# Performance work log

Measured on AMD Instinct MI355X. Metric: run time of the kernel, lower is better.

Reference implementation:

```python
import jax, jax.numpy as jnp
import numpy as np

N_NODES = 100000
N_EDGES = 1000000
N_GRAPHS = 2048
IN_DIM, HIDDEN, OUT_DIM = 5, 64, 128


def setup_inputs() -> dict:
    key = jax.random.key(0)
    ks = jax.random.split(key, 12)
    x = jax.random.normal(ks[0], (N_NODES, IN_DIM), dtype=jnp.float32)
    edge_index = jax.random.randint(ks[1], (2, N_EDGES), 0, N_NODES, dtype=jnp.int64)
    batch = jnp.sort(jax.random.randint(ks[2], (N_NODES,), 0, N_GRAPHS, dtype=jnp.int64))
    def lin(k, fan_in, fan_out):
        bound = 1.0 / np.sqrt(fan_in)
        kw, kb = jax.random.split(k)
        W = jax.random.uniform(kw, (fan_in, fan_out), jnp.float32, -bound, bound)
        b = jax.random.uniform(kb, (fan_out,), jnp.float32, -bound, bound)
        return W, b
    W1, b1 = lin(ks[3], IN_DIM, HIDDEN)
    W2, b2 = lin(ks[4], HIDDEN, HIDDEN)
    W3, b3 = lin(ks[5], HIDDEN, HIDDEN)
    W4, b4 = lin(ks[6], HIDDEN, OUT_DIM)
    return {"x": x, "edge_index": edge_index, "batch": batch,
            "W1": W1, "b1": b1, "W2": W2, "b2": b2,
            "W3": W3, "b3": b3, "W4": W4, "b4": b4}


def _gcn_conv(x, W, b, src, dst, norm, n):
    # h = x W; message from src, scaled by symmetric norm, scattered to dst
    h = x @ W                                   # [N, F]
    msg = h[src] * norm[:, None]                # [E+N, F] gather
    agg = jax.ops.segment_sum(msg, dst, num_segments=n)  # scatter-add
    return agg + b


def reference(x, edge_index, batch, W1, b1, W2, b2, W3, b3, W4, b4):
    n = x.shape[0]
    loop = jnp.arange(n, dtype=edge_index.dtype)
    # GCN with self-loops: src -> dst aggregation, D^-1/2 A_hat D^-1/2 norm
    src = jnp.concatenate([edge_index[0], loop])
    dst = jnp.concatenate([edge_index[1], loop])
    deg = jax.ops.segment_sum(jnp.ones_like(dst, dtype=x.dtype), dst, num_segments=n)
    dinv = jnp.where(deg > 0, jax.lax.rsqrt(jnp.maximum(deg, 1.0)), 0.0)
    norm = dinv[src] * dinv[dst]                # [E+N]

    h = jax.nn.relu(_gcn_conv(x, W1, b1, src, dst, norm, n))
    h = jax.nn.relu(_gcn_conv(h, W2, b2, src, dst, norm, n))

    # global mean pool per graph
    sums = jax.ops.segment_sum(h, batch, num_segments=N_GRAPHS)      # [G, F]
    cnts = jax.ops.segment_sum(jnp.ones((n,), h.dtype), batch, num_segments=N_GRAPHS)
    pooled = sums / jnp.maximum(cnts, 1.0)[:, None]

    # MLP head
    z = jax.nn.relu(pooled @ W3 + b3)
    return z @ W4 + b4
```

## Files before the change

kernel.cpp:

```cpp
#include <hip/hip_runtime.h>
#include <hip/hip_fp16.h>

#define N_NODES  100000
#define N_EDGES  1000000
#define N_GRAPHS 2048
#define IN_DIM   5
#define HIDDEN   64
#define OUT_DIM  128
#define CAP      32
#define NA       512
#define PART     256
#define NBIN     391
#define CAPBIN   4096
#define LSTR     72
#define MAXN     192
#define NSTG     96
#define EPT      8

typedef _Float16 f16x8 __attribute__((ext_vector_type(8)));
typedef float    f32x4 __attribute__((ext_vector_type(4)));


__global__ void __launch_bounds__(256) k_part2(
        const int* __restrict__ src, const int* __restrict__ dst,
        const int* __restrict__ batch, int* __restrict__ gcursor,
        int* __restrict__ epart, int* __restrict__ gs) {
    __shared__ int h[NBIN];
    __shared__ int off[NBIN];
    int t = threadIdx.x, b = blockIdx.x;

    int gid = b * 256 + t;
    if (gid < N_NODES) {
        int bi = batch[gid];
        int bp = (gid == 0) ? -1 : batch[gid - 1];
        for (int g = bp + 1; g <= bi; g++) gs[g] = gid;
        if (gid == N_NODES - 1)
            for (int g = bi + 1; g <= N_GRAPHS; g++) gs[g] = N_NODES;
    }

    for (int i = t; i < NBIN; i += 256) h[i] = 0;
    __syncthreads();
    int ebin[EPT], epay[EPT];
    int ebase = b * 256 + t;
#pragma unroll
    for (int i = 0; i < EPT; i++) {
        int e = ebase + i * (NA * 256);
        ebin[i] = -1;
        if (e < N_EDGES) {
            int d = dst[e];
            ebin[i] = d >> 8;
            epay[i] = ((d & (PART - 1)) << 17) | src[e];
            atomicAdd(&h[ebin[i]], 1);
        }
    }
    __syncthreads();
    for (int i = t; i < NBIN; i += 256) {
        int c = h[i];
        int base = c ? atomicAdd(&gcursor[i], c) : 0;
        off[i] = i * CAPBIN + base;
    }
    __syncthreads();
#pragma unroll
    for (int i = 0; i < EPT; i++) {
        if (ebin[i] >= 0) {
            int pos = atomicAdd(&off[ebin[i]], 1);
            if (pos < (ebin[i] + 1) * CAPBIN)
                epart[pos] = epay[i];
        }
    }
}

__global__ void __launch_bounds__(256) k_build(
        const int* __restrict__ epart, const int* __restrict__ bincnt,
        const float* __restrict__ x, int* __restrict__ cnt, int* __restrict__ bkt,
        float* __restrict__ dinv, __half* __restrict__ xs) {
    __shared__ int lcnt[PART];
    __shared__ int lrows[PART * CAP];
    int t = threadIdx.x, b = blockIdx.x;
    int base = b * PART;
    for (int i = t; i < PART; i += 256) lcnt[i] = 0;
    __syncthreads();
    int estart = b * CAPBIN;
    int eend = estart + min(bincnt[b], CAPBIN);
    for (int i = estart + t; i < eend; i += 256) {
        int ed = epart[i];
        int ln = ed >> 17;
        int c = atomicAdd(&lcnt[ln], 1);
        if (c < CAP) lrows[ln * CAP + c] = ed & 0x1FFFF;
    }
    __syncthreads();
    int gbase = base * CAP;
    int lim = min(PART * CAP, N_NODES * CAP - gbase);
    for (int i = t; i < lim; i += 256) bkt[gbase + i] = lrows[i];
    for (int n = t; n < PART; n += 256) {
        int g = base + n;
        if (g < N_NODES) {
            int c = lcnt[n];
            cnt[g] = c;
            float d = rsqrtf(1.0f + (float)c);
            dinv[g] = d;
            union { __half h[8]; float4 f4; } u;
#pragma unroll
            for (int k = 0; k < 8; k++)
                u.h[k] = __float2half((k < IN_DIM) ? x[g * IN_DIM + k] * d : 0.0f);
            ((float4*)xs)[g] = u.f4;
        }
    }
}

__global__ void __launch_bounds__(256) k_g5l12(
        const int* __restrict__ cnt, const int* __restrict__ bkt,
        const __half* __restrict__ xs,
        const float* __restrict__ W1, const float* __restrict__ b1,
        const float* __restrict__ W2, const float* __restrict__ dinv,
        __half* __restrict__ hs2h) {
    __shared__ __align__(16) _Float16 lh1[64 * LSTR];
    __shared__ __align__(16) _Float16 lw2[64 * LSTR];
    __shared__ float la5[64][8];
    __shared__ unsigned short ordn[64];
    __shared__ int dsh[CAP + 1];
    __shared__ int sdeg[64];
    int tid = threadIdx.x;
    int w = tid >> 6, l = tid & 63;
    int nodeBase = blockIdx.x * 64;

#pragma unroll
    for (int i = 0; i < 4; i++) {
        int idx = tid + i * 256;
        float4 wv = ((const float4*)W2)[idx];
        int k = idx >> 4, n4 = (idx & 15) * 4;
        lw2[(n4 + 0) * LSTR + k] = (_Float16)wv.x;
        lw2[(n4 + 1) * LSTR + k] = (_Float16)wv.y;
        lw2[(n4 + 2) * LSTR + k] = (_Float16)wv.z;
        lw2[(n4 + 3) * LSTR + k] = (_Float16)wv.w;
    }

    int* sbkt5 = (int*)lh1;
    {
        const int4* gb = (const int4*)(bkt + (size_t)nodeBase * CAP);
        int4* sb = (int4*)sbkt5;
        int lim4 = min(64, N_NODES - nodeBase) * (CAP / 4);
        for (int i = tid; i < lim4; i += 256) sb[i] = gb[i];
    }

    if (tid <= CAP) dsh[tid] = 0;
    __syncthreads();
    int mydeg = 0;
    if (tid < 64) {
        int g = nodeBase + tid;
        mydeg = (g < N_NODES) ? min(cnt[g], CAP) : 0;
        sdeg[tid] = mydeg;
        atomicAdd(&dsh[mydeg], 1);
    }
    __syncthreads();
    if (tid < 64) {
        int orig = (tid <= CAP) ? dsh[tid] : 0;
        int v = orig;
#pragma unroll
        for (int off = 1; off < 64; off <<= 1) {
            int u = __shfl_up(v, off);
            if (tid >= off) v += u;
        }
        if (tid <= CAP) dsh[tid] = v - orig;
    }
    __syncthreads();
    if (tid < 64) { int pos = atomicAdd(&dsh[mydeg], 1); ordn[pos] = tid; }
    __syncthreads();

    {
        int g4 = l >> 2, l4 = l & 3;
        int lnm = ordn[w * 16 + g4];
        int g = nodeBase + lnm;
        float s0 = 0.f, s1 = 0.f, s2 = 0.f, s3 = 0.f;
        float s4 = 0.f, s5 = 0.f, s6 = 0.f, s7 = 0.f;
        if (g < N_NODES) {
            const float4* XS4 = (const float4*)xs;
            int len = sdeg[lnm];
            const int* row = sbkt5 + lnm * CAP;
#define XACC(r) { const __half2* hp_ = (const __half2*)&(r);                   \
            float2 u0_ = __half22float2(hp_[0]), u1_ = __half22float2(hp_[1]); \
            float2 u2_ = __half22float2(hp_[2]), u3_ = __half22float2(hp_[3]); \
            s0 += u0_.x; s1 += u0_.y; s2 += u1_.x; s3 += u1_.y;                \
            s4 += u2_.x; s5 += u2_.y; s6 += u3_.x; s7 += u3_.y; }
            int e = l4;
            for (; e + 4 < len; e += 8) {
                float4 r0 = XS4[row[e]];
                float4 r1 = XS4[row[e + 4]];
                XACC(r0); XACC(r1);
            }
            if (e < len) { float4 r0 = XS4[row[e]]; XACC(r0); }
            if (l4 == 0) { float4 rs = XS4[g]; XACC(rs); }
#undef XACC
        }
#pragma unroll
        for (int m = 1; m <= 2; m <<= 1) {
            s0 += __shfl_xor(s0, m); s1 += __shfl_xor(s1, m);
            s2 += __shfl_xor(s2, m); s3 += __shfl_xor(s3, m);
            s4 += __shfl_xor(s4, m); s5 += __shfl_xor(s5, m);
            s6 += __shfl_xor(s6, m); s7 += __shfl_xor(s7, m);
        }
        if (l4 == 0) {
            float d = (g < N_NODES) ? dinv[g] : 0.f;
            la5[lnm][0] = s0 * d; la5[lnm][1] = s1 * d;
            la5[lnm][2] = s2 * d; la5[lnm][3] = s3 * d;
            la5[lnm][4] = s4 * d; la5[lnm][5] = s5 * d;
            la5[lnm][6] = s6 * d; la5[lnm][7] = s7 * d;
        }
    }
    __syncthreads();

    int f = l;
    float b1v = b1[f];
    float w1v[IN_DIM];
#pragma unroll
    for (int k = 0; k < IN_DIM; k++) w1v[k] = W1[k * HIDDEN + f];
    for (int i = 0; i < 16; i++) {
        int ln = w * 16 + i;
        float t1 = b1v;
#pragma unroll
        for (int k = 0; k < IN_DIM; k++)
            t1 += la5[ln][k] * w1v[k];
        lh1[ln * LSTR + f] = (_Float16)fmaxf(t1, 0.f);
    }
    __syncthreads();

    int quad = l >> 4, m16 = l & 15;
    f32x4 acc0 = {0.f, 0.f, 0.f, 0.f};
    f32x4 acc1 = {0.f, 0.f, 0.f, 0.f};
    f32x4 acc2 = {0.f, 0.f, 0.f, 0.f};
    f32x4 acc3 = {0.f, 0.f, 0.f, 0.f};
#pragma unroll
    for (int kc = 0; kc < 2; kc++) {
        f16x8 a = *(const f16x8*)&lh1[(w * 16 + m16) * LSTR + kc * 32 + quad * 8];
        f16x8 b0 = *(const f16x8*)&lw2[(0 * 16 + m16) * LSTR + kc * 32 + quad * 8];
        f16x8 b1f = *(const f16x8*)&lw2[(1 * 16 + m16) * LSTR + kc * 32 + quad * 8];
        f16x8 b2 = *(const f16x8*)&lw2[(2 * 16 + m16) * LSTR + kc * 32 + quad * 8];
        f16x8 b3 = *(const f16x8*)&lw2[(3 * 16 + m16) * LSTR + kc * 32 + quad * 8];
        acc0 = __builtin_amdgcn_mfma_f32_16x16x32_f16(a, b0, acc0, 0, 0, 0);
        acc1 = __builtin_amdgcn_mfma_f32_16x16x32_f16(a, b1f, acc1, 0, 0, 0);
        acc2 = __builtin_amdgcn_mfma_f32_16x16x32_f16(a, b2, acc2, 0, 0, 0);
        acc3 = __builtin_amdgcn_mfma_f32_16x16x32_f16(a, b3, acc3, 0, 0, 0);
    }
#pragma unroll
    for (int i = 0; i < 4; i++) {
        int g = nodeBase + w * 16 + quad * 4 + i;
        if (g >= N_NODES) continue;
        float dv = dinv[g];
        __half* row = hs2h + (size_t)g * HIDDEN + m16;
        row[0]  = __float2half(acc0[i] * dv);
        row[16] = __float2half(acc1[i] * dv);
        row[32] = __float2half(acc2[i] * dv);
        row[48] = __float2half(acc3[i] * dv);
    }
}

__global__ void __launch_bounds__(256) k_g2ph(
        const int* __restrict__ cnt, const int* __restrict__ bkt,
        const __half* __restrict__ hs2h, const float* __restrict__ dinv,
        const int* __restrict__ gs, const float* __restrict__ b2,
        const float* __restrict__ W3, const float* __restrict__ b3,
        const float* __restrict__ W4, const float* __restrict__ b4,
        float* __restrict__ out) {
    __shared__ __align__(16) int sbkt[NSTG][CAP];
    __shared__ int   scnt[NSTG];
    __shared__ float sdinv[NSTG];
    __shared__ float pool[4][HIDDEN];
    __shared__ float gp[HIDDEN];
    __shared__ float gz[HIDDEN];
    __shared__ unsigned short ord[MAXN];
    __shared__ int dsh[CAP + 1];
    int g = blockIdx.x, tid = threadIdx.x;
    int grp = tid >> 3, l8 = tid & 7;
    int w = tid >> 6;
    int s = gs[g], e = gs[g + 1];
    int n = e - s;
    int nst = min(n, NSTG);
    bool dosort = (n <= MAXN);

    {
        const int4* gb = (const int4*)(bkt + (size_t)s * CAP);
        int4* sb = (int4*)&sbkt[0][0];
        int tot = nst * (CAP / 4);
        for (int i = tid; i < tot; i += 256) sb[i] = gb[i];
    }
    for (int i = tid; i < nst; i += 256) {
        scnt[i]  = min(cnt[s + i], CAP);
        sdinv[i] = dinv[s + i];
    }
    if (tid <= CAP) dsh[tid] = 0;
    __syncthreads();

    int mydeg = 0;
    if (dosort && tid < n) {
        mydeg = (tid < nst) ? scnt[tid] : min(cnt[s + tid], CAP);
        atomicAdd(&dsh[mydeg], 1);
    }
    __syncthreads();
    if (tid < 64) {
        int orig = (tid <= CAP) ? dsh[tid] : 0;
        int v = orig;
#pragma unroll
        for (int off = 1; off < 64; off <<= 1) {
            int u = __shfl_up(v, off);
            if (tid >= off) v += u;
        }
        if (tid <= CAP) dsh[tid] = v - orig;
    }
    __syncthreads();
    if (dosort && tid < n) { int pos = atomicAdd(&dsh[mydeg], 1); ord[pos] = tid; }
    __syncthreads();

    const float4* H16 = (const float4*)hs2h;
    float4 b2a = ((const float4*)b2)[l8 * 2];
    float4 b2b = ((const float4*)b2)[l8 * 2 + 1];
    float p0 = 0.f, p1 = 0.f, p2 = 0.f, p3 = 0.f;
    float p4 = 0.f, p5 = 0.f, p6 = 0.f, p7 = 0.f;

#define ACCA(r) { const __half2* hp_ = (const __half2*)&(r);               \
        float2 u0_ = __half22float2(hp_[0]), u1_ = __half22float2(hp_[1]); \
        float2 u2_ = __half22float2(hp_[2]), u3_ = __half22float2(hp_[3]); \
        a0 += u0_.x; a1 += u0_.y; a2 += u1_.x; a3 += u1_.y;                \
        a4 += u2_.x; a5 += u2_.y; a6 += u3_.x; a7 += u3_.y; }
#define ACCC(r) { const __half2* hp_ = (const __half2*)&(r);               \
        float2 u0_ = __half22float2(hp_[0]), u1_ = __half22float2(hp_[1]); \
        float2 u2_ = __half22float2(hp_[2]), u3_ = __half22float2(hp_[3]); \
        c0 += u0_.x; c1 += u0_.y; c2 += u1_.x; c3 += u1_.y;                \
        c4 += u2_.x; c5 += u2_.y; c6 += u3_.x; c7 += u3_.y; }

#define NODE_BODY(ROW, LEN, DV, NODE)                                      \
    {                                                                      \
        float a0 = 0.f, a1 = 0.f, a2 = 0.f, a3 = 0.f;                      \
        float a4 = 0.f, a5 = 0.f, a6 = 0.f, a7 = 0.f;                      \
        float c0 = 0.f, c1 = 0.f, c2 = 0.f, c3 = 0.f;                      \
        float c4 = 0.f, c5 = 0.f, c6 = 0.f, c7 = 0.f;                      \
        int ee = 0;                                                        \
        for (; ee + 8 <= (LEN); ee += 8) {                                 \
            int4 i0 = *(const int4*)&(ROW)[ee];                            \
            int4 i1 = *(const int4*)&(ROW)[ee + 4];                        \
            float4 r0 = H16[(size_t)i0.x * 8 + l8];                        \
            float4 r1 = H16[(size_t)i0.y * 8 + l8];                        \
            float4 r2 = H16[(size_t)i0.z * 8 + l8];                        \
            float4 r3 = H16[(size_t)i0.w * 8 + l8];                        \
            float4 r4 = H16[(size_t)i1.x * 8 + l8];                        \
            float4 r5 = H16[(size_t)i1.y * 8 + l8];                        \
            float4 r6 = H16[(size_t)i1.z * 8 + l8];                        \
            float4 r7 = H16[(size_t)i1.w * 8 + l8];                        \
            ACCA(r0); ACCC(r1); ACCA(r2); ACCC(r3);                        \
            ACCA(r4); ACCC(r5); ACCA(r6); ACCC(r7);                        \
        }                                                                  \
        if (ee + 4 <= (LEN)) {                                             \
            int4 i0 = *(const int4*)&(ROW)[ee];                            \
            float4 r0 = H16[(size_t)i0.x * 8 + l8];                        \
            float4 r1 = H16[(size_t)i0.y * 8 + l8];                        \
            float4 r2 = H16[(size_t)i0.z * 8 + l8];                        \
            float4 r3 = H16[(size_t)i0.w * 8 + l8];                        \
            ACCA(r0); ACCC(r1); ACCA(r2); ACCC(r3);                        \
            ee += 4;                                                       \
        }                                                                  \
        for (; ee < (LEN); ee++) {                                         \
            float4 r0 = H16[(size_t)(ROW)[ee] * 8 + l8];                   \
            ACCA(r0);                                                      \
        }                                                                  \
        { float4 rs = H16[(size_t)(NODE) * 8 + l8]; ACCA(rs); }            \
        float dv_ = (DV);                                                  \
        p0 += fmaxf((a0 + c0) * dv_ + b2a.x, 0.f);                         \
        p1 += fmaxf((a1 + c1) * dv_ + b2a.y, 0.f);                         \
        p2 += fmaxf((a2 + c2) * dv_ + b2a.z, 0.f);                         \
        p3 += fmaxf((a3 + c3) * dv_ + b2a.w, 0.f);                         \
        p4 += fmaxf((a4 + c4) * dv_ + b2b.x, 0.f);                         \
        p5 += fmaxf((a5 + c5) * dv_ + b2b.y, 0.f);                         \
        p6 += fmaxf((a6 + c6) * dv_ + b2b.z, 0.f);                         \
        p7 += fmaxf((a7 + c7) * dv_ + b2b.w, 0.f);                         \
    }

    if (n <= NSTG) {
        for (int r = grp; r < n; r += 32) {
            int ln = dosort ? (int)ord[r] : r;
            const int* row = &sbkt[ln][0];
            NODE_BODY(row, scnt[ln], sdinv[ln], s + ln);
        }
    } else {
        for (int r = grp; r < n; r += 32) {
            int ln = dosort ? (int)ord[r] : r;
            int node = s + ln;
            const int* row = bkt + (size_t)node * CAP;
            NODE_BODY(row, min(cnt[node], CAP), dinv[node], node);
        }
    }
#undef NODE_BODY
#undef ACCA
#undef ACCC
#pragma unroll
    for (int m = 8; m <= 32; m <<= 1) {
        p0 += __shfl_xor(p0, m); p1 += __shfl_xor(p1, m);
        p2 += __shfl_xor(p2, m); p3 += __shfl_xor(p3, m);
        p4 += __shfl_xor(p4, m); p5 += __shfl_xor(p5, m);
        p6 += __shfl_xor(p6, m); p7 += __shfl_xor(p7, m);
    }
    if ((tid & 63) < 8) {
        float* pw = &pool[w][l8 * 8];
        pw[0] = p0; pw[1] = p1; pw[2] = p2; pw[3] = p3;
        pw[4] = p4; pw[5] = p5; pw[6] = p6; pw[7] = p7;
    }
    __syncthreads();
    if (tid < HIDDEN) {
        float inv = 1.0f / fmaxf((float)n, 1.0f);
        gp[tid] = (pool[0][tid] + pool[1][tid] + pool[2][tid] + pool[3][tid]) * inv;
    }
    __syncthreads();
    if (tid < HIDDEN) {
        float t = b3[tid];
#pragma unroll 8
        for (int k = 0; k < HIDDEN; k++) t += gp[k] * W3[k * HIDDEN + tid];
        gz[tid] = fmaxf(t, 0.f);
    }
    __syncthreads();
    if (tid < OUT_DIM) {
        float t = b4[tid];
#pragma unroll 8
        for (int k = 0; k < HIDDEN; k++) t += gz[k] * W4[k * OUT_DIM + tid];
        out[(size_t)g * OUT_DIM + tid] = t;
    }
}

extern "C" void kernel_launch(void* const* d_in, const int* in_sizes, int n_in,
                              void* d_out, int out_size, void* d_ws, size_t ws_size,
                              hipStream_t stream) {
    const float* x  = (const float*)d_in[0];
    const int*   ei = (const int*)d_in[1];
    const int*   batch = (const int*)d_in[2];
    const float* W1 = (const float*)d_in[3];
    const float* b1 = (const float*)d_in[4];
    const float* W2 = (const float*)d_in[5];
    const float* b2 = (const float*)d_in[6];
    const float* W3 = (const float*)d_in[7];
    const float* b3 = (const float*)d_in[8];
    const float* W4 = (const float*)d_in[9];
    const float* b4 = (const float*)d_in[10];
    float* out = (float*)d_out;

    const int* src = ei;
    const int* dst = ei + N_EDGES;

    char* wp = (char*)d_ws;
    auto carve = [&](size_t bytes) -> void* {
        void* p = (void*)wp;
        wp += (bytes + 255) & ~(size_t)255;
        return p;
    };
    int*    cnt     = (int*)carve((size_t)N_NODES * sizeof(int));
    int*    bkt     = (int*)carve((size_t)N_NODES * CAP * sizeof(int));
    float*  dinv    = (float*)carve((size_t)N_NODES * sizeof(float));
    __half* hs2h    = (__half*)carve((size_t)N_NODES * HIDDEN * sizeof(__half));
    __half* xs      = (__half*)carve((size_t)N_NODES * 8 * sizeof(__half));
    int*    epart   = (int*)carve((size_t)NBIN * CAPBIN * sizeof(int));
    int*    gs      = (int*)carve((size_t)(N_GRAPHS + 1) * sizeof(int));
    int*    gcursor = (int*)carve((size_t)NBIN * sizeof(int));

    hipMemsetAsync(gcursor, 0, (size_t)NBIN * sizeof(int), stream);
    k_part2<<<NA, 256, 0, stream>>>(src, dst, batch, gcursor, epart, gs);
    k_build<<<NBIN, 256, 0, stream>>>(epart, gcursor, x, cnt, bkt, dinv, xs);
    k_g5l12<<<(N_NODES + 63) / 64, 256, 0, stream>>>(cnt, bkt, xs, W1, b1, W2,
                                                     dinv, hs2h);
    k_g2ph<<<N_GRAPHS, 256, 0, stream>>>(cnt, bkt, hs2h, dinv, gs, b2,
                                         W3, b3, W4, b4, out);
}
```

Baseline: 158.7 us.

## Split build blocks in half and schedule pooling blocks largest-graph-first

The build kernel now launches twice as many blocks. Each block handles half of a 256-node partition, which halves shared memory per block and should raise occupancy. Each half rescans the full edge bin and filters to its own nodes. Block 0 also counting-sorts the graphs by node count in descending order into a permutation. The pooling/MLP kernel then takes its graph from that permutation so the largest graphs start first, which should reduce tail imbalance. The costs are the duplicated edge-bin reads and serial sorting work inside one build block.

```diff
diff --git a/kernel.cpp b/kernel.cpp
--- a/kernel.cpp
+++ b/kernel.cpp
@@ -16,6 +16,7 @@
 #define MAXN     192
 #define NSTG     96
 #define EPT      8
+#define HPART    128
 
 typedef _Float16 f16x8 __attribute__((ext_vector_type(8)));
 typedef float    f32x4 __attribute__((ext_vector_type(4)));
@@ -73,26 +74,53 @@
 __global__ void __launch_bounds__(256) k_build(
         const int* __restrict__ epart, const int* __restrict__ bincnt,
         const float* __restrict__ x, int* __restrict__ cnt, int* __restrict__ bkt,
-        float* __restrict__ dinv, __half* __restrict__ xs) {
-    __shared__ int lcnt[PART];
-    __shared__ int lrows[PART * CAP];
-    int t = threadIdx.x, b = blockIdx.x;
-    int base = b * PART;
-    for (int i = t; i < PART; i += 256) lcnt[i] = 0;
+        float* __restrict__ dinv, __half* __restrict__ xs,
+        const int* __restrict__ gs, int* __restrict__ gperm) {
+    __shared__ int lcnt[HPART];
+    __shared__ int lrows[HPART * CAP];
+    __shared__ int ghist[MAXN + 1];
+    int t = threadIdx.x, bb = blockIdx.x;
+    int b = bb >> 1, half = bb & 1;
+    int lbase = half * HPART;
+    int base = b * PART + lbase;
+
+    if (bb == 0) {
+        for (int i = t; i <= MAXN; i += 256) ghist[i] = 0;
+        __syncthreads();
+        for (int g = t; g < N_GRAPHS; g += 256) {
+            int n = gs[g + 1] - gs[g];
+            atomicAdd(&ghist[MAXN - min(n, MAXN)], 1);
+        }
+        __syncthreads();
+        if (t == 0) {
+            int acc = 0;
+            for (int i = 0; i <= MAXN; i++) { int c = ghist[i]; ghist[i] = acc; acc += c; }
+        }
+        __syncthreads();
+        for (int g = t; g < N_GRAPHS; g += 256) {
+            int n = gs[g + 1] - gs[g];
+            int pos = atomicAdd(&ghist[MAXN - min(n, MAXN)], 1);
+            gperm[pos] = g;
+        }
+    }
+
+    for (int i = t; i < HPART; i += 256) lcnt[i] = 0;
     __syncthreads();
     int estart = b * CAPBIN;
     int eend = estart + min(bincnt[b], CAPBIN);
     for (int i = estart + t; i < eend; i += 256) {
         int ed = epart[i];
-        int ln = ed >> 17;
-        int c = atomicAdd(&lcnt[ln], 1);
-        if (c < CAP) lrows[ln * CAP + c] = ed & 0x1FFFF;
+        int lh = (ed >> 17) - lbase;
+        if ((unsigned)lh < (unsigned)HPART) {
+            int c = atomicAdd(&lcnt[lh], 1);
+            if (c < CAP) lrows[lh * CAP + c] = ed & 0x1FFFF;
+        }
     }
     __syncthreads();
     int gbase = base * CAP;
-    int lim = min(PART * CAP, N_NODES * CAP - gbase);
+    int lim = min(HPART * CAP, N_NODES * CAP - gbase);
     for (int i = t; i < lim; i += 256) bkt[gbase + i] = lrows[i];
-    for (int n = t; n < PART; n += 256) {
+    for (int n = t; n < HPART; n += 256) {
         int g = base + n;
         if (g < N_NODES) {
             int c = lcnt[n];
@@ -257,7 +285,8 @@
 __global__ void __launch_bounds__(256) k_g2ph(
         const int* __restrict__ cnt, const int* __restrict__ bkt,
         const __half* __restrict__ hs2h, const float* __restrict__ dinv,
-        const int* __restrict__ gs, const float* __restrict__ b2,
+        const int* __restrict__ gs, const int* __restrict__ gperm,
+        const float* __restrict__ b2,
         const float* __restrict__ W3, const float* __restrict__ b3,
         const float* __restrict__ W4, const float* __restrict__ b4,
         float* __restrict__ out) {
@@ -269,7 +298,8 @@
     __shared__ float gz[HIDDEN];
     __shared__ unsigned short ord[MAXN];
     __shared__ int dsh[CAP + 1];
-    int g = blockIdx.x, tid = threadIdx.x;
+    int g = gperm[blockIdx.x];
+    int tid = threadIdx.x;
     int grp = tid >> 3, l8 = tid & 7;
     int w = tid >> 6;
     int s = gs[g], e = gs[g + 1];
@@ -456,12 +486,14 @@
     int*    epart   = (int*)carve((size_t)NBIN * CAPBIN * sizeof(int));
     int*    gs      = (int*)carve((size_t)(N_GRAPHS + 1) * sizeof(int));
     int*    gcursor = (int*)carve((size_t)NBIN * sizeof(int));
+    int*    gperm   = (int*)carve((size_t)N_GRAPHS * sizeof(int));
 
     hipMemsetAsync(gcursor, 0, (size_t)NBIN * sizeof(int), stream);
     k_part2<<<NA, 256, 0, stream>>>(src, dst, batch, gcursor, epart, gs);
-    k_build<<<NBIN, 256, 0, stream>>>(epart, gcursor, x, cnt, bkt, dinv, xs);
+    k_build<<<NBIN * 2, 256, 0, stream>>>(epart, gcursor, x, cnt, bkt, dinv, xs,
+                                          gs, gperm);
     k_g5l12<<<(N_NODES + 63) / 64, 256, 0, stream>>>(cnt, bkt, xs, W1, b1, W2,
                                                      dinv, hs2h);
-    k_g2ph<<<N_GRAPHS, 256, 0, stream>>>(cnt, bkt, hs2h, dinv, gs, b2,
+    k_g2ph<<<N_GRAPHS, 256, 0, stream>>>(cnt, bkt, hs2h, dinv, gs, gperm, b2,
                                          W3, b3, W4, b4, out);
 }
```

Measured after the change: 161.0 us. No clear change (+1.5%).
